# Kernel tuning notes

Measured on AMD Instinct MI355X. Metric: run time of the kernel, lower is better.

Reference implementation:

```python
import jax, jax.numpy as jnp
import numpy as np

N_ATOMS = 100000
N_PAIRS = 6400000
BOX_L = 100.0  # Angstrom, cubic box


def setup_inputs() -> dict:
    key = jax.random.key(0)
    k1, k2, k3, k4, k5 = jax.random.split(key, 5)
    coords = jax.random.uniform(k1, (N_ATOMS, 3), dtype=jnp.float32) * BOX_L
    # build pairs with guaranteed i != j (avoids dr == 0 -> inf/nan)
    i = jax.random.randint(k2, (N_PAIRS,), 0, N_ATOMS)
    off = jax.random.randint(k3, (N_PAIRS,), 1, N_ATOMS)
    pairs = jnp.stack([i, (i + off) % N_ATOMS], axis=1)
    box = jnp.eye(3, dtype=jnp.float32) * BOX_L
    sigma = jax.random.uniform(k4, (N_ATOMS,), dtype=jnp.float32) * 1.0 + 2.5
    epsilon = jax.random.uniform(k5, (N_ATOMS,), dtype=jnp.float32) * 0.4 + 0.05
    return {"coords": coords, "pairs": pairs, "box": box,
            "sigma": sigma, "epsilon": epsilon, "cutoff": 12}


def reference(coords, pairs, box, sigma, epsilon, cutoff):
    i, j = pairs[:, 0], pairs[:, 1]
    dr_vecs = coords[i] - coords[j]                 # [P,3] gather + diff
    box_inv = jnp.linalg.inv(box)                   # [3,3]
    ds = dr_vecs @ box_inv                          # fractional coords
    ds = ds - jnp.floor(ds + 0.5)                   # PBC minimum-image fold
    dr_pbc = ds @ box                               # back to cartesian
    dr = jnp.linalg.norm(dr_pbc, axis=1)            # [P]
    mask = dr <= cutoff
    sigma_ij = (sigma[i] + sigma[j]) * 0.5          # Lorentz mixing
    epsilon_ij = jnp.sqrt(epsilon[i] * epsilon[j])  # Berthelot mixing
    tmp = (sigma_ij / dr) ** 6
    ene = 4.0 * epsilon_ij * tmp * (tmp - 1.0)
    return jnp.sum(ene * mask)
```

## Files before the change

### kernel.cpp

```cpp
#include <hip/hip_runtime.h>
#include <hip/hip_fp16.h>

#define BLOCK 256
#define MAIN_BLOCKS_NOF 4096
#define FBLOCK 1024
#define FGRID 256
#define NWAVES (FBLOCK / 64)
#define QCAP 256

__global__ void lj_prep_kernel(const float* __restrict__ coords,
                               const float* __restrict__ sigma,
                               const float* __restrict__ eps,
                               const float* __restrict__ box,
                               float4* __restrict__ table,
                               unsigned char* __restrict__ cellg,
                               float* __restrict__ out,
                               int n_atoms) {
    int i = blockIdx.x * blockDim.x + threadIdx.x;
    if (i == 0) out[0] = 0.0f;
    if (i >= n_atoms) return;
    float x = coords[3 * i + 0];
    float y = coords[3 * i + 1];
    float z = coords[3 * i + 2];
    float s  = sigma[i];
    float se = sqrtf(eps[i]);
    unsigned pack = (unsigned)__half_as_ushort(__float2half(s)) |
                    ((unsigned)__half_as_ushort(__float2half(se)) << 16);
    table[i] = make_float4(x, y, z, __uint_as_float(pack));

    float L0 = box[0], L1 = box[4], L2 = box[8];
    int cx = min((int)(x * (8.0f / L0)), 7); cx = max(cx, 0);
    int cy = min((int)(y * (8.0f / L1)), 7); cy = max(cy, 0);
    int cz = min((int)(z * (4.0f / L2)), 3); cz = max(cz, 0);
    cellg[i] = (unsigned char)(cx | (cy << 3) | (cz << 6));
}

__device__ __forceinline__ float lj_energy(float4 pi, float4 pj,
                                           float L0, float L1, float L2,
                                           float b0, float b1, float b2,
                                           float c2) {
    float dx = pi.x - pj.x;
    float dy = pi.y - pj.y;
    float dz = pi.z - pj.z;
    float sx = dx * b0; sx -= floorf(sx + 0.5f); dx = sx * L0;
    float sy = dy * b1; sy -= floorf(sy + 0.5f); dy = sy * L1;
    float sz = dz * b2; sz -= floorf(sz + 0.5f); dz = sz * L2;
    float r2 = dx * dx + dy * dy + dz * dz;

    unsigned packi = __float_as_uint(pi.w);
    unsigned packj = __float_as_uint(pj.w);
    float si  = __half2float(__ushort_as_half((unsigned short)(packi & 0xffffu)));
    float sj  = __half2float(__ushort_as_half((unsigned short)(packj & 0xffffu)));
    float sei = __half2float(__ushort_as_half((unsigned short)(packi >> 16)));
    float sej = __half2float(__ushort_as_half((unsigned short)(packj >> 16)));

    float sij   = (si + sj) * 0.5f;
    float epsij = sei * sej;
    float ratio = (sij * sij) / r2;
    float t     = ratio * ratio * ratio;
    float e     = 4.0f * epsij * t * (t - 1.0f);
    return (r2 <= c2) ? e : 0.0f;
}

__device__ __forceinline__ bool cell_near(unsigned ci, unsigned cj) {
    unsigned dcx = (ci - cj) & 7u;
    unsigned dcy = ((ci >> 3) - (cj >> 3)) & 7u;
    unsigned dcz = ((ci >> 6) - (cj >> 6)) & 3u;
    return (dcx <= 1u || dcx == 7u) &&
           (dcy <= 1u || dcy == 7u) &&
           (dcz <= 1u || dcz == 3u);
}

__global__ __launch_bounds__(FBLOCK) void lj_main_filtered(
        const int4* __restrict__ pairs4,
        const int2* __restrict__ pairs2,
        const float4* __restrict__ table,
        const unsigned char* __restrict__ cellg,
        const float* __restrict__ box,
        const int* __restrict__ cutoff,
        float* __restrict__ out,
        int n_atoms, int n4, int n_pairs, int qoff) {
    extern __shared__ unsigned char lds[];
    unsigned char* cellLds = lds;
    int lane = threadIdx.x & 63;
    int wid  = threadIdx.x >> 6;
    int2* queue = (int2*)(lds + qoff) + wid * QCAP;

    int n16 = n_atoms >> 4;
    const uint4* src = (const uint4*)cellg;
    uint4* dst = (uint4*)cellLds;
    for (int k = threadIdx.x; k < n16; k += blockDim.x) dst[k] = src[k];
    for (int k = (n16 << 4) + threadIdx.x; k < n_atoms; k += blockDim.x)
        cellLds[k] = cellg[k];
    __syncthreads();

    const float L0 = box[0], L1 = box[4], L2 = box[8];
    const float b0 = 1.0f / L0, b1 = 1.0f / L1, b2 = 1.0f / L2;
    const float c  = (float)cutoff[0];
    const float c2 = c * c;
    const bool use_filter = (c <= L0 * 0.125f) && (c <= L1 * 0.125f) &&
                            (c <= L2 * 0.25f);

    float acc = 0.0f;
    int qcount = 0, head = 0;

    long base = ((long)blockIdx.x * NWAVES + wid) * 64;
    long step = (long)gridDim.x * NWAVES * 64;

    bool v = (base + lane) < n4;
    int4 pp = v ? pairs4[base + lane] : make_int4(0, 0, 0, 0);

    while (base < n4) {
        long nbase = base + step;
        bool vn = (nbase + lane) < n4;
        int4 ppn = vn ? pairs4[nbase + lane] : make_int4(0, 0, 0, 0);

        bool near0 = v && (!use_filter || cell_near(cellLds[pp.x], cellLds[pp.y]));
        unsigned long long bal0 = __ballot(near0);
        int pos0 = (int)__popcll(bal0 & ((1ull << lane) - 1ull));
        if (near0) queue[(head + qcount + pos0) & (QCAP - 1)] = make_int2(pp.x, pp.y);
        qcount += (int)__popcll(bal0);

        bool near1 = v && (!use_filter || cell_near(cellLds[pp.z], cellLds[pp.w]));
        unsigned long long bal1 = __ballot(near1);
        int pos1 = (int)__popcll(bal1 & ((1ull << lane) - 1ull));
        if (near1) queue[(head + qcount + pos1) & (QCAP - 1)] = make_int2(pp.z, pp.w);
        qcount += (int)__popcll(bal1);

        while (qcount >= 64) {
            int2 e = queue[(head + lane) & (QCAP - 1)];
            float4 pi = table[e.x];
            float4 pj = table[e.y];
            acc += lj_energy(pi, pj, L0, L1, L2, b0, b1, b2, c2);
            head = (head + 64) & (QCAP - 1);
            qcount -= 64;
        }

        base = nbase; pp = ppn; v = vn;
    }
    if (lane < qcount) {
        int2 e = queue[(head + lane) & (QCAP - 1)];
        float4 pi = table[e.x];
        float4 pj = table[e.y];
        acc += lj_energy(pi, pj, L0, L1, L2, b0, b1, b2, c2);
    }
    if (blockIdx.x == 0 && threadIdx.x == 0 && (n_pairs & 1)) {
        int2 e = pairs2[n_pairs - 1];
        acc += lj_energy(table[e.x], table[e.y], L0, L1, L2, b0, b1, b2, c2);
    }

    for (int off = 32; off > 0; off >>= 1)
        acc += __shfl_down(acc, off, 64);

    __shared__ float wsum[NWAVES];
    if (lane == 0) wsum[wid] = acc;
    __syncthreads();
    if (threadIdx.x == 0) {
        float s = 0.0f;
        for (int w = 0; w < NWAVES; w++) s += wsum[w];
        atomicAdd(out, s);
    }
}

__global__ __launch_bounds__(BLOCK) void lj_main_kernel(
        const int2* __restrict__ pairs,
        const float4* __restrict__ table,
        const float* __restrict__ box,
        const int* __restrict__ cutoff,
        float* __restrict__ out,
        int n_pairs) {
    const float L0 = box[0], L1 = box[4], L2 = box[8];
    const float b0 = 1.0f / L0, b1 = 1.0f / L1, b2 = 1.0f / L2;
    const float c  = (float)cutoff[0];
    const float c2 = c * c;

    float acc = 0.0f;
    int tid = blockIdx.x * blockDim.x + threadIdx.x;
    int stride = gridDim.x * blockDim.x;
    for (int p = tid; p < n_pairs; p += stride) {
        int2 ij = pairs[p];
        float4 pi = table[ij.x];
        float4 pj = table[ij.y];
        acc += lj_energy(pi, pj, L0, L1, L2, b0, b1, b2, c2);
    }
    for (int off = 32; off > 0; off >>= 1)
        acc += __shfl_down(acc, off, 64);
    __shared__ float wsum[BLOCK / 64];
    int lane = threadIdx.x & 63;
    int wid  = threadIdx.x >> 6;
    if (lane == 0) wsum[wid] = acc;
    __syncthreads();
    if (threadIdx.x == 0) {
        float s = 0.0f;
        for (int w = 0; w < BLOCK / 64; w++) s += wsum[w];
        atomicAdd(out, s);
    }
}

extern "C" void kernel_launch(void* const* d_in, const int* in_sizes, int n_in,
                              void* d_out, int out_size, void* d_ws, size_t ws_size,
                              hipStream_t stream) {
    const float* coords = (const float*)d_in[0];
    const int*   pairsi = (const int*)d_in[1];
    const float* box    = (const float*)d_in[2];
    const float* sigma  = (const float*)d_in[3];
    const float* eps    = (const float*)d_in[4];
    const int*   cutoff = (const int*)d_in[5];
    int n_atoms = in_sizes[0] / 3;
    int n_pairs = in_sizes[1] / 2;
    float* out = (float*)d_out;

    size_t table_bytes = ((size_t)n_atoms * sizeof(float4) + 255) & ~(size_t)255;
    size_t cell_bytes  = (size_t)n_atoms;
    float4* table = (float4*)d_ws;
    unsigned char* cellg = (unsigned char*)d_ws + table_bytes;

    int qoff = (n_atoms + 15) & ~15;
    int shmem = qoff + NWAVES * QCAP * (int)sizeof(int2);

    lj_prep_kernel<<<(n_atoms + 255) / 256, 256, 0, stream>>>(
        coords, sigma, eps, box, table, cellg, out, n_atoms);

    bool can_filter = (ws_size >= table_bytes + cell_bytes) &&
                      (shmem <= 160 * 1024 - 1024);

    if (can_filter) {
        static bool attr_set = false;
        if (!attr_set) {
            hipFuncSetAttribute((const void*)lj_main_filtered,
                                hipFuncAttributeMaxDynamicSharedMemorySize,
                                shmem);
            attr_set = true;
        }
        lj_main_filtered<<<FGRID, FBLOCK, shmem, stream>>>(
            (const int4*)pairsi, (const int2*)pairsi, table, cellg, box,
            cutoff, out, n_atoms, n_pairs / 2, n_pairs, qoff);
    } else {
        lj_main_kernel<<<MAIN_BLOCKS_NOF, BLOCK, 0, stream>>>(
            (const int2*)pairsi, table, box, cutoff, out, n_pairs);
    }
}
```

Baseline: 104.5 us.

## Drop LDS cell-table staging, read cells from global, raise grid and occupancy

Removes the per-block copy of the 100KB cell-index table into LDS and reads cell bytes straight from global memory, which should be L2/cache resident. LDS then holds only the per-wave queues, so more blocks can sit on each CU, and the grid is doubled to 512 blocks. The change also uses mbcnt intrinsics for the lane prefix count and 32-bit indices. The trade-off is that each cell lookup becomes a scattered global byte load in place of an LDS read.

```diff
diff --git a/kernel.cpp b/kernel.cpp
--- a/kernel.cpp
+++ b/kernel.cpp
@@ -4,7 +4,7 @@
 #define BLOCK 256
 #define MAIN_BLOCKS_NOF 4096
 #define FBLOCK 1024
-#define FGRID 256
+#define FGRID 512
 #define NWAVES (FBLOCK / 64)
 #define QCAP 256
 
@@ -71,7 +71,13 @@
            (dcz <= 1u || dcz == 3u);
 }
 
-__global__ __launch_bounds__(FBLOCK) void lj_main_filtered(
+__device__ __forceinline__ int prefix_cnt(unsigned long long bal) {
+    return (int)__builtin_amdgcn_mbcnt_hi(
+        (unsigned)(bal >> 32),
+        __builtin_amdgcn_mbcnt_lo((unsigned)bal, 0u));
+}
+
+__global__ __launch_bounds__(FBLOCK, 8) void lj_main_filtered(
         const int4* __restrict__ pairs4,
         const int2* __restrict__ pairs2,
         const float4* __restrict__ table,
@@ -79,20 +85,11 @@
         const float* __restrict__ box,
         const int* __restrict__ cutoff,
         float* __restrict__ out,
-        int n_atoms, int n4, int n_pairs, int qoff) {
-    extern __shared__ unsigned char lds[];
-    unsigned char* cellLds = lds;
+        int n_atoms, int n4, int n_pairs) {
+    __shared__ int2 queue_s[NWAVES][QCAP];
     int lane = threadIdx.x & 63;
     int wid  = threadIdx.x >> 6;
-    int2* queue = (int2*)(lds + qoff) + wid * QCAP;
-
-    int n16 = n_atoms >> 4;
-    const uint4* src = (const uint4*)cellg;
-    uint4* dst = (uint4*)cellLds;
-    for (int k = threadIdx.x; k < n16; k += blockDim.x) dst[k] = src[k];
-    for (int k = (n16 << 4) + threadIdx.x; k < n_atoms; k += blockDim.x)
-        cellLds[k] = cellg[k];
-    __syncthreads();
+    int2* queue = queue_s[wid];
 
     const float L0 = box[0], L1 = box[4], L2 = box[8];
     const float b0 = 1.0f / L0, b1 = 1.0f / L1, b2 = 1.0f / L2;
@@ -104,26 +101,31 @@
     float acc = 0.0f;
     int qcount = 0, head = 0;
 
-    long base = ((long)blockIdx.x * NWAVES + wid) * 64;
-    long step = (long)gridDim.x * NWAVES * 64;
+    int base = (blockIdx.x * NWAVES + wid) * 64;
+    int step = (int)gridDim.x * NWAVES * 64;
 
     bool v = (base + lane) < n4;
     int4 pp = v ? pairs4[base + lane] : make_int4(0, 0, 0, 0);
 
     while (base < n4) {
-        long nbase = base + step;
+        int nbase = base + step;
         bool vn = (nbase + lane) < n4;
         int4 ppn = vn ? pairs4[nbase + lane] : make_int4(0, 0, 0, 0);
 
-        bool near0 = v && (!use_filter || cell_near(cellLds[pp.x], cellLds[pp.y]));
+        unsigned ca0 = cellg[pp.x];
+        unsigned cb0 = cellg[pp.y];
+        unsigned ca1 = cellg[pp.z];
+        unsigned cb1 = cellg[pp.w];
+
+        bool near0 = v && (!use_filter || cell_near(ca0, cb0));
         unsigned long long bal0 = __ballot(near0);
-        int pos0 = (int)__popcll(bal0 & ((1ull << lane) - 1ull));
+        int pos0 = prefix_cnt(bal0);
         if (near0) queue[(head + qcount + pos0) & (QCAP - 1)] = make_int2(pp.x, pp.y);
         qcount += (int)__popcll(bal0);
 
-        bool near1 = v && (!use_filter || cell_near(cellLds[pp.z], cellLds[pp.w]));
+        bool near1 = v && (!use_filter || cell_near(ca1, cb1));
         unsigned long long bal1 = __ballot(near1);
-        int pos1 = (int)__popcll(bal1 & ((1ull << lane) - 1ull));
+        int pos1 = prefix_cnt(bal1);
         if (near1) queue[(head + qcount + pos1) & (QCAP - 1)] = make_int2(pp.z, pp.w);
         qcount += (int)__popcll(bal1);
 
@@ -215,26 +217,15 @@
     float4* table = (float4*)d_ws;
     unsigned char* cellg = (unsigned char*)d_ws + table_bytes;
 
-    int qoff = (n_atoms + 15) & ~15;
-    int shmem = qoff + NWAVES * QCAP * (int)sizeof(int2);
-
     lj_prep_kernel<<<(n_atoms + 255) / 256, 256, 0, stream>>>(
         coords, sigma, eps, box, table, cellg, out, n_atoms);
 
-    bool can_filter = (ws_size >= table_bytes + cell_bytes) &&
-                      (shmem <= 160 * 1024 - 1024);
+    bool can_filter = (ws_size >= table_bytes + cell_bytes);
 
     if (can_filter) {
-        static bool attr_set = false;
-        if (!attr_set) {
-            hipFuncSetAttribute((const void*)lj_main_filtered,
-                                hipFuncAttributeMaxDynamicSharedMemorySize,
-                                shmem);
-            attr_set = true;
-        }
-        lj_main_filtered<<<FGRID, FBLOCK, shmem, stream>>>(
+        lj_main_filtered<<<FGRID, FBLOCK, 0, stream>>>(
             (const int4*)pairsi, (const int2*)pairsi, table, cellg, box,
-            cutoff, out, n_atoms, n_pairs / 2, n_pairs, qoff);
+            cutoff, out, n_atoms, n_pairs / 2, n_pairs);
     } else {
         lj_main_kernel<<<MAIN_BLOCKS_NOF, BLOCK, 0, stream>>>(
             (const int2*)pairsi, table, box, cutoff, out, n_pairs);
```

Measured after the change: 134.9 us. 1.29x slower.

## Replace wave-level compaction queue with direct divergent evaluation over contiguous chunks

Applied to the files above, without the earlier changes.

Removes the per-wave LDS queue that compacted cell-near pairs via ballot/popcount before evaluating energies, and instead evaluates near pairs directly under a lane predicate. Each wave now walks a contiguous chunk of pairs rather than a grid-strided range. This drops queue writes/reads and ballot overhead and shrinks LDS use, but lanes in the energy path are mostly idle because near pairs are sparse, so gathers and math run at low lane utilization.

```diff
diff --git a/kernel.cpp b/kernel.cpp
--- a/kernel.cpp
+++ b/kernel.cpp
@@ -6,7 +6,6 @@
 #define FBLOCK 1024
 #define FGRID 256
 #define NWAVES (FBLOCK / 64)
-#define QCAP 256
 
 __global__ void lj_prep_kernel(const float* __restrict__ coords,
                                const float* __restrict__ sigma,
@@ -71,7 +70,7 @@
            (dcz <= 1u || dcz == 3u);
 }
 
-__global__ __launch_bounds__(FBLOCK) void lj_main_filtered(
+__global__ __launch_bounds__(FBLOCK) void lj_main_direct(
         const int4* __restrict__ pairs4,
         const int2* __restrict__ pairs2,
         const float4* __restrict__ table,
@@ -79,12 +78,11 @@
         const float* __restrict__ box,
         const int* __restrict__ cutoff,
         float* __restrict__ out,
-        int n_atoms, int n4, int n_pairs, int qoff) {
+        int n_atoms, int n4, int n_pairs) {
     extern __shared__ unsigned char lds[];
     unsigned char* cellLds = lds;
     int lane = threadIdx.x & 63;
     int wid  = threadIdx.x >> 6;
-    int2* queue = (int2*)(lds + qoff) + wid * QCAP;
 
     int n16 = n_atoms >> 4;
     const uint4* src = (const uint4*)cellg;
@@ -102,47 +100,38 @@
                             (c <= L2 * 0.25f);
 
     float acc = 0.0f;
-    int qcount = 0, head = 0;
-
-    long base = ((long)blockIdx.x * NWAVES + wid) * 64;
-    long step = (long)gridDim.x * NWAVES * 64;
-
-    bool v = (base + lane) < n4;
-    int4 pp = v ? pairs4[base + lane] : make_int4(0, 0, 0, 0);
-
-    while (base < n4) {
-        long nbase = base + step;
-        bool vn = (nbase + lane) < n4;
-        int4 ppn = vn ? pairs4[nbase + lane] : make_int4(0, 0, 0, 0);
-
-        bool near0 = v && (!use_filter || cell_near(cellLds[pp.x], cellLds[pp.y]));
-        unsigned long long bal0 = __ballot(near0);
-        int pos0 = (int)__popcll(bal0 & ((1ull << lane) - 1ull));
-        if (near0) queue[(head + qcount + pos0) & (QCAP - 1)] = make_int2(pp.x, pp.y);
-        qcount += (int)__popcll(bal0);
-
-        bool near1 = v && (!use_filter || cell_near(cellLds[pp.z], cellLds[pp.w]));
-        unsigned long long bal1 = __ballot(near1);
-        int pos1 = (int)__popcll(bal1 & ((1ull << lane) - 1ull));
-        if (near1) queue[(head + qcount + pos1) & (QCAP - 1)] = make_int2(pp.z, pp.w);
-        qcount += (int)__popcll(bal1);
-
-        while (qcount >= 64) {
-            int2 e = queue[(head + lane) & (QCAP - 1)];
-            float4 pi = table[e.x];
-            float4 pj = table[e.y];
+
+    int nW = FGRID * NWAVES;
+    int per_wave = (n4 + nW - 1) / nW;
+    int gwid  = blockIdx.x * NWAVES + wid;
+    int p     = gwid * per_wave;
+    int pend  = min(p + per_wave, n4);
+
+    bool v = (p + lane) < pend;
+    int4 pp = v ? pairs4[p + lane] : make_int4(0, 0, 0, 0);
+
+    while (p < pend) {
+        int np = p + 64;
+        bool vn = (np + lane) < pend;
+        int4 ppn = vn ? pairs4[np + lane] : make_int4(0, 0, 0, 0);
+
+        unsigned ca = cellLds[pp.x];
+        unsigned cb = cellLds[pp.y];
+        unsigned cc = cellLds[pp.z];
+        unsigned cd = cellLds[pp.w];
+
+        if (v && (!use_filter || cell_near(ca, cb))) {
+            float4 pi = table[pp.x];
+            float4 pj = table[pp.y];
             acc += lj_energy(pi, pj, L0, L1, L2, b0, b1, b2, c2);
-            head = (head + 64) & (QCAP - 1);
-            qcount -= 64;
         }
-
-        base = nbase; pp = ppn; v = vn;
-    }
-    if (lane < qcount) {
-        int2 e = queue[(head + lane) & (QCAP - 1)];
-        float4 pi = table[e.x];
-        float4 pj = table[e.y];
-        acc += lj_energy(pi, pj, L0, L1, L2, b0, b1, b2, c2);
+        if (v && (!use_filter || cell_near(cc, cd))) {
+            float4 pi = table[pp.z];
+            float4 pj = table[pp.w];
+            acc += lj_energy(pi, pj, L0, L1, L2, b0, b1, b2, c2);
+        }
+
+        p = np; pp = ppn; v = vn;
     }
     if (blockIdx.x == 0 && threadIdx.x == 0 && (n_pairs & 1)) {
         int2 e = pairs2[n_pairs - 1];
@@ -215,8 +204,7 @@
     float4* table = (float4*)d_ws;
     unsigned char* cellg = (unsigned char*)d_ws + table_bytes;
 
-    int qoff = (n_atoms + 15) & ~15;
-    int shmem = qoff + NWAVES * QCAP * (int)sizeof(int2);
+    int shmem = (n_atoms + 15) & ~15;
 
     lj_prep_kernel<<<(n_atoms + 255) / 256, 256, 0, stream>>>(
         coords, sigma, eps, box, table, cellg, out, n_atoms);
@@ -227,14 +215,14 @@
     if (can_filter) {
         static bool attr_set = false;
         if (!attr_set) {
-            hipFuncSetAttribute((const void*)lj_main_filtered,
+            hipFuncSetAttribute((const void*)lj_main_direct,
                                 hipFuncAttributeMaxDynamicSharedMemorySize,
                                 shmem);
             attr_set = true;
         }
-        lj_main_filtered<<<FGRID, FBLOCK, shmem, stream>>>(
+        lj_main_direct<<<FGRID, FBLOCK, shmem, stream>>>(
             (const int4*)pairsi, (const int2*)pairsi, table, cellg, box,
-            cutoff, out, n_atoms, n_pairs / 2, n_pairs, qoff);
+            cutoff, out, n_atoms, n_pairs / 2, n_pairs);
     } else {
         lj_main_kernel<<<MAIN_BLOCKS_NOF, BLOCK, 0, stream>>>(
             (const int2*)pairsi, table, box, cutoff, out, n_pairs);
```

Measured after the change: 116.8 us. 11.8% more time.
